# Optimization experiments

Measured on AMD Instinct MI355X. Metric: run time of the kernel, lower is better.

## Reference

```python
import jax, jax.numpy as jnp
import numpy as np

DECAY = 0.99
EPS = 1e-06


def setup_inputs() -> dict:
    key = jax.random.key(0)
    k1, k2, k3 = jax.random.split(key, 3)
    B, S, D, K = 8, 8192, 256, 2048
    x = jax.random.normal(k1, (B, S, D), dtype=jnp.float32)
    embed = jax.random.normal(k2, (K, D), dtype=jnp.float32)
    cluster_size = jnp.ones((K,), dtype=jnp.float32)
    embed_avg = jax.random.normal(k3, (K, D), dtype=jnp.float32)
    return {"x": x, "embed": embed, "cluster_size": cluster_size, "embed_avg": embed_avg}


def reference(x, embed, cluster_size, embed_avg):
    # x: [B, S, D]; embed/embed_avg: [K, D]; cluster_size: [K]
    B, S, D = x.shape
    K = embed.shape[0]
    xf = x.reshape(-1, D)  # [N, D]
    dist = (
        jnp.sum(xf * xf, axis=1, keepdims=True)
        - 2.0 * (xf @ embed.T)
        + jnp.sum(embed * embed, axis=1)
    )
    embed_ind_flat = jnp.argmin(dist, axis=-1)  # [N]
    quantize = embed[embed_ind_flat].reshape(B, S, D)
    embed_ind = embed_ind_flat.reshape(B, S)

    # EMA updates (training branch). one_hot.sum(0) == per-code counts,
    # one_hot.T @ x == per-code feature sums; use segment_sum (no NxK one-hot).
    counts = jax.ops.segment_sum(
        jnp.ones((B * S,), dtype=jnp.float32), embed_ind_flat, num_segments=K
    )
    embed_sum = jax.ops.segment_sum(xf, embed_ind_flat, num_segments=K)  # [K, D]
    new_cluster_size = cluster_size * DECAY + (1.0 - DECAY) * counts
    new_embed_avg = embed_avg * DECAY + (1.0 - DECAY) * embed_sum
    total = new_cluster_size.sum()
    smoothed = (new_cluster_size + EPS) / (total + EPS * K) * total  # laplace smoothing
    new_embed = new_embed_avg / smoothed[:, None]
    return quantize, embed_ind, new_cluster_size, new_embed_avg, new_embed
```

## Files before the change

kernel.cpp:

```cpp
#include <hip/hip_runtime.h>
#include <hip/hip_fp16.h>
#include <float.h>

#define DECAY 0.99f
#define OMD   0.01f
#define EPSF  1e-6f

constexpr int Bb = 8, Ss = 8192, Dd = 256, Kk = 2048;
constexpr int Nn = Bb * Ss;

constexpr long OUT_QUANT = 0;
constexpr long OUT_IND   = (long)Nn * Dd;
constexpr long OUT_NCS   = OUT_IND + Nn;
constexpr long OUT_NEA   = OUT_NCS + Kk;
constexpr long OUT_NE    = OUT_NEA + (long)Kk * Dd;

constexpr long WS_COUNTS = 0;
constexpr long WS_TOTAL  = 2048;
constexpr long WS_EE     = 2112;
constexpr long WS_BIG    = 4160;
constexpr int  PARTS     = 8;
constexpr int  CODES     = 8;

typedef __attribute__((ext_vector_type(8))) short short8;
typedef __attribute__((ext_vector_type(8))) _Float16 half8;
typedef __attribute__((ext_vector_type(4))) float floatx4;

#define WINDOW 0.5f

__device__ __forceinline__ void gl_lds(const ushort* g, ushort* l)
{
    __builtin_amdgcn_global_load_lds(
        (const __attribute__((address_space(1))) void*)g,
        (__attribute__((address_space(3))) void*)l,
        16, 0, 0);
}

__device__ __forceinline__ ushort f2h(float v)
{
    __half h = __float2half(v);
    return *(ushort*)&h;
}

__global__ __launch_bounds__(256) void convert_x_kernel(
    const float* __restrict__ x, ushort* __restrict__ x_h)
{
    long base = ((long)blockIdx.x * 256 + threadIdx.x) * 8;
    float4 a = *(const float4*)&x[base];
    float4 b = *(const float4*)&x[base + 4];
    short8 h;
    h[0] = (short)f2h(a.x); h[1] = (short)f2h(a.y);
    h[2] = (short)f2h(a.z); h[3] = (short)f2h(a.w);
    h[4] = (short)f2h(b.x); h[5] = (short)f2h(b.y);
    h[6] = (short)f2h(b.z); h[7] = (short)f2h(b.w);
    *(short8*)&x_h[base] = h;
}

__global__ __launch_bounds__(256) void convert_e_kernel(
    const float* __restrict__ embed, ushort* __restrict__ e_h,
    float* __restrict__ ee)
{
    int row  = blockIdx.x * 4 + (threadIdx.x >> 6);
    int lane = threadIdx.x & 63;
    long base = (long)row * Dd + lane * 4;
    float4 v = *(const float4*)&embed[base];
    float s = v.x * v.x + v.y * v.y + v.z * v.z + v.w * v.w;
    ushort4 h;
    h.x = f2h(v.x); h.y = f2h(v.y); h.z = f2h(v.z); h.w = f2h(v.w);
    *(ushort4*)&e_h[base] = h;
    #pragma unroll
    for (int off = 32; off >= 1; off >>= 1)
        s += __shfl_xor(s, off, 64);
    if (lane == 0) ee[row] = s;
}

__global__ __attribute__((amdgpu_waves_per_eu(2, 2))) __launch_bounds__(256)
void pass1_kernel(
    const ushort* __restrict__ x_h, const ushort* __restrict__ e_h,
    const float* __restrict__ ee, float* __restrict__ ind_out,
    int* __restrict__ qbase)
{
    __shared__ __attribute__((aligned(16))) ushort ah[128 * 64];
    __shared__ __attribute__((aligned(16))) ushort bh[256 * 64];
    __shared__ float  redv[2][128];
    __shared__ float  red2[2][128];
    __shared__ int    redi[2][128];

    const int tid  = threadIdx.x;
    const int lane = tid & 63;
    const int quad = lane >> 4;
    const int l15  = lane & 15;
    const int w    = tid >> 6;
    const int wy   = w >> 1;
    const int wx   = w & 1;
    const long row0 = (long)blockIdx.x * 128;

    const int rloc   = lane >> 3;
    const int cchunk = (lane & 7) ^ rloc;
    const int gcoff  = rloc * 256 + cchunk * 8;

    const int s7 = l15 & 7;

    float bestv[16], best2v[16];
    int   besti[16];
    #pragma unroll
    for (int i = 0; i < 16; ++i) { bestv[i] = FLT_MAX; best2v[i] = FLT_MAX; besti[i] = 0; }

    for (int ct = 0; ct < Kk / 256; ++ct) {
        floatx4 acc[4][8];
        #pragma unroll
        for (int rt = 0; rt < 4; ++rt)
            #pragma unroll
            for (int jt = 0; jt < 8; ++jt)
                acc[rt][jt] = (floatx4){0.f, 0.f, 0.f, 0.f};

        const long brow = (long)ct * 256;

        for (int kc = 0; kc < 4; ++kc) {
            const int kcol = kc * 64;

            __syncthreads();
            #pragma unroll
            for (int i = 0; i < 4; ++i) {
                const int u = w + 4 * i;
                gl_lds(&x_h[((row0 + u * 8) << 8) + kcol + gcoff], &ah[u * 512]);
            }
            #pragma unroll
            for (int i = 0; i < 8; ++i) {
                const int u = w + 4 * i;
                gl_lds(&e_h[((brow + u * 8) << 8) + kcol + gcoff], &bh[u * 512]);
            }
            __syncthreads();

            #pragma unroll
            for (int ks = 0; ks < 2; ++ks) {
                const int cterm = (((ks * 4 + quad) ^ s7) * 8);
                half8 af[4];
                #pragma unroll
                for (int rt = 0; rt < 4; ++rt)
                    af[rt] = *(const half8*)&ah[((wy * 64 + rt * 16 + l15) << 6) + cterm];
                #pragma unroll
                for (int jt = 0; jt < 8; ++jt) {
                    half8 bf = *(const half8*)&bh[((wx * 128 + jt * 16 + l15) << 6) + cterm];
                    #pragma unroll
                    for (int rt = 0; rt < 4; ++rt)
                        acc[rt][jt] = __builtin_amdgcn_mfma_f32_16x16x32_f16(
                            af[rt], bf, acc[rt][jt], 0, 0, 0);
                }
            }
        }

        #pragma unroll
        for (int jt = 0; jt < 8; ++jt) {
            int c = ct * 256 + wx * 128 + jt * 16 + l15;
            float eec = ee[c];
            #pragma unroll
            for (int rt = 0; rt < 4; ++rt) {
                #pragma unroll
                for (int reg = 0; reg < 4; ++reg) {
                    float s = eec - 2.0f * acc[rt][jt][reg];
                    int slot = rt * 4 + reg;
                    if (s < bestv[slot]) {
                        best2v[slot] = bestv[slot];
                        bestv[slot] = s; besti[slot] = c;
                    } else {
                        best2v[slot] = fminf(best2v[slot], s);
                    }
                }
            }
        }
    }

    #pragma unroll
    for (int slot = 0; slot < 16; ++slot) {
        float bv = bestv[slot]; int bi = besti[slot]; float b2 = best2v[slot];
        #pragma unroll
        for (int off = 8; off >= 1; off >>= 1) {
            float ov  = __shfl_xor(bv, off, 16);
            int   oi  = __shfl_xor(bi, off, 16);
            float ov2 = __shfl_xor(b2, off, 16);
            float nm2 = fminf(fminf(b2, ov2), fmaxf(bv, ov));
            if (ov < bv) { bv = ov; bi = oi; }
            b2 = nm2;
        }
        bestv[slot] = bv; besti[slot] = bi; best2v[slot] = b2;
    }

    if (l15 == 0) {
        #pragma unroll
        for (int rt = 0; rt < 4; ++rt)
            #pragma unroll
            for (int reg = 0; reg < 4; ++reg) {
                int rloc2 = wy * 64 + rt * 16 + quad * 4 + reg;
                int slot = rt * 4 + reg;
                redv[wx][rloc2] = bestv[slot];
                red2[wx][rloc2] = best2v[slot];
                redi[wx][rloc2] = besti[slot];
            }
    }
    __syncthreads();
    if (tid < 128) {
        float v0 = redv[0][tid], v1 = redv[1][tid];
        float s0 = red2[0][tid], s1 = red2[1][tid];
        float m1, m2; int mi;
        if (v0 <= v1) { m1 = v0; mi = redi[0][tid]; m2 = fminf(fminf(s0, s1), v1); }
        else          { m1 = v1; mi = redi[1][tid]; m2 = fminf(fminf(s0, s1), v0); }
        long rowAbs = row0 + tid;
        ind_out[rowAbs] = (float)mi;
        if (m2 - m1 <= WINDOW) {
            int q = atomicAdd(qbase, 1);
            qbase[1 + q] = (int)rowAbs;
        }
    }
}

constexpr int RB = 8;
__global__ __launch_bounds__(256) void pass2_kernel(
    const float* __restrict__ x, const float* __restrict__ embed,
    const float* __restrict__ ee, const int* __restrict__ qbase,
    float* __restrict__ ind_out)
{
    __shared__ float xs[RB][256];
    __shared__ float sv[RB][256];
    __shared__ int   si[RB][256];
    const int tid = threadIdx.x;
    const int count = qbase[0];

    for (int q0 = blockIdx.x * RB; q0 < count; q0 += gridDim.x * RB) {
        const int nr = (count - q0 < RB) ? (count - q0) : RB;
        __syncthreads();
        for (int r = 0; r < nr; ++r)
            xs[r][tid] = x[(long)qbase[1 + q0 + r] * Dd + tid];
        __syncthreads();

        float bv[RB]; int bi[RB];
        #pragma unroll
        for (int r = 0; r < RB; ++r) { bv[r] = FLT_MAX; bi[r] = 0; }

        for (int i = 0; i < Kk / 256; ++i) {
            const int c = i * 256 + tid;
            const float4* er = (const float4*)&embed[(long)c * Dd];
            float dot[RB];
            #pragma unroll
            for (int r = 0; r < RB; ++r) dot[r] = 0.0f;
            for (int d = 0; d < Dd / 4; ++d) {
                float4 e4 = er[d];
                #pragma unroll
                for (int r = 0; r < RB; ++r) {
                    float4 x4 = *(const float4*)&xs[r][d * 4];
                    dot[r] += e4.x * x4.x + e4.y * x4.y + e4.z * x4.z + e4.w * x4.w;
                }
            }
            float eec = ee[c];
            #pragma unroll
            for (int r = 0; r < RB; ++r) {
                float s = eec - 2.0f * dot[r];
                if (s < bv[r]) { bv[r] = s; bi[r] = c; }
            }
        }

        #pragma unroll
        for (int r = 0; r < RB; ++r) { sv[r][tid] = bv[r]; si[r][tid] = bi[r]; }
        __syncthreads();
        for (int off = 128; off >= 1; off >>= 1) {
            if (tid < off) {
                #pragma unroll
                for (int r = 0; r < RB; ++r) {
                    float v2 = sv[r][tid + off]; int i2 = si[r][tid + off];
                    if (v2 < sv[r][tid] || (v2 == sv[r][tid] && i2 < si[r][tid])) {
                        sv[r][tid] = v2; si[r][tid] = i2;
                    }
                }
            }
            __syncthreads();
        }
        if (tid < nr)
            ind_out[qbase[1 + q0 + tid]] = (float)si[tid][0];
        __syncthreads();
    }
}

__global__ __launch_bounds__(256) void quant_gather_kernel(
    const float* __restrict__ embed, const float* __restrict__ ind_f,
    float* __restrict__ quant)
{
    long row  = (long)blockIdx.x * 4 + (threadIdx.x >> 6);
    int  lane = threadIdx.x & 63;
    int  idx  = (int)ind_f[row];
    float4 ev = *(const float4*)&embed[(long)idx * Dd + lane * 4];
    *(float4*)&quant[row * Dd + lane * 4] = ev;
}

template <int USE_ATOMIC>
__global__ __launch_bounds__(256) void segsum_kernel(
    const float* __restrict__ x, const float* __restrict__ ind_f,
    float* __restrict__ dst, float* __restrict__ counts)
{
    __shared__ float part[CODES][4][256];
    __shared__ float cnt_l[CODES][4];
    const int tid  = threadIdx.x;
    const int w    = tid >> 6;
    const int lane = tid & 63;
    const int k0   = (blockIdx.x >> 3) * CODES;
    const int s    = blockIdx.x & 7;

    constexpr int STRIP = Nn / PARTS;
    constexpr int WAVE_ROWS = STRIP / 4;
    const int base0 = s * STRIP + w * WAVE_ROWS;

    float4 acc[CODES];
    int    cnt[CODES];
    #pragma unroll
    for (int c = 0; c < CODES; ++c) { acc[c] = (float4){0.f,0.f,0.f,0.f}; cnt[c] = 0; }

    for (int win = 0; win < WAVE_ROWS; win += 64) {
        int idx = (int)ind_f[base0 + win + lane];
        unsigned rel = (unsigned)(idx - k0);
        unsigned long long m = __ballot(rel < (unsigned)CODES);
        while (m) {
            int l = __ffsll((unsigned long long)m) - 1;
            m &= m - 1;
            int code = __shfl((int)rel, l, 64);
            long row = base0 + win + l;
            float4 v = *(const float4*)&x[row * Dd + lane * 4];
            switch (code) {
                case 0: acc[0].x+=v.x; acc[0].y+=v.y; acc[0].z+=v.z; acc[0].w+=v.w; cnt[0]++; break;
                case 1: acc[1].x+=v.x; acc[1].y+=v.y; acc[1].z+=v.z; acc[1].w+=v.w; cnt[1]++; break;
                case 2: acc[2].x+=v.x; acc[2].y+=v.y; acc[2].z+=v.z; acc[2].w+=v.w; cnt[2]++; break;
                case 3: acc[3].x+=v.x; acc[3].y+=v.y; acc[3].z+=v.z; acc[3].w+=v.w; cnt[3]++; break;
                case 4: acc[4].x+=v.x; acc[4].y+=v.y; acc[4].z+=v.z; acc[4].w+=v.w; cnt[4]++; break;
                case 5: acc[5].x+=v.x; acc[5].y+=v.y; acc[5].z+=v.z; acc[5].w+=v.w; cnt[5]++; break;
                case 6: acc[6].x+=v.x; acc[6].y+=v.y; acc[6].z+=v.z; acc[6].w+=v.w; cnt[6]++; break;
                case 7: acc[7].x+=v.x; acc[7].y+=v.y; acc[7].z+=v.z; acc[7].w+=v.w; cnt[7]++; break;
            }
        }
    }

    #pragma unroll
    for (int c = 0; c < CODES; ++c) {
        *(float4*)&part[c][w][lane * 4] = acc[c];
        if (lane == 0) cnt_l[c][w] = (float)cnt[c];
    }
    __syncthreads();

    #pragma unroll
    for (int c = 0; c < CODES; ++c) {
        float sum = part[c][0][tid] + part[c][1][tid] + part[c][2][tid] + part[c][3][tid];
        if (USE_ATOMIC) {
            if (sum != 0.0f) atomicAdd(&dst[(long)(k0 + c) * Dd + tid], sum);
        } else {
            dst[((long)s * Kk + (k0 + c)) * Dd + tid] = sum;
        }
    }
    if (tid < CODES)
        atomicAdd(&counts[k0 + tid],
                  cnt_l[tid][0] + cnt_l[tid][1] + cnt_l[tid][2] + cnt_l[tid][3]);
}

__global__ __launch_bounds__(256) void ema_cs_kernel(
    const float* __restrict__ cs, const float* __restrict__ counts,
    float* __restrict__ ncs, float* __restrict__ total_ws)
{
    __shared__ float red[256];
    int tid = threadIdx.x;
    float s = 0.0f;
    #pragma unroll
    for (int i = 0; i < 8; ++i) {
        int k = tid + i * 256;
        float v = cs[k] * DECAY + OMD * counts[k];
        ncs[k] = v;
        s += v;
    }
    red[tid] = s;
    __syncthreads();
    #pragma unroll
    for (int off = 128; off >= 1; off >>= 1) {
        if (tid < off) red[tid] += red[tid + off];
        __syncthreads();
    }
    if (tid == 0) total_ws[0] = red[0];
}

__global__ __launch_bounds__(256) void nea_ne_kernel(
    const float* __restrict__ ea, const float* __restrict__ partials,
    int nparts, const float* __restrict__ ncs, const float* __restrict__ total_ws,
    float* __restrict__ nea, float* __restrict__ ne)
{
    long g = ((long)blockIdx.x * 256 + threadIdx.x) * 4;
    int  k = (int)(g >> 8);
    int  d = (int)(g & 255);

    float4 sv = {0.f, 0.f, 0.f, 0.f};
    for (int p = 0; p < nparts; ++p) {
        float4 pv = *(const float4*)&partials[((long)p * Kk + k) * Dd + d];
        sv.x += pv.x; sv.y += pv.y; sv.z += pv.z; sv.w += pv.w;
    }

    float4 av = *(const float4*)&ea[g];
    float4 out_nea;
    out_nea.x = av.x * DECAY + OMD * sv.x;
    out_nea.y = av.y * DECAY + OMD * sv.y;
    out_nea.z = av.z * DECAY + OMD * sv.z;
    out_nea.w = av.w * DECAY + OMD * sv.w;
    *(float4*)&nea[g] = out_nea;

    float total = total_ws[0];
    float sm = (ncs[k] + EPSF) / (total + EPSF * (float)Kk) * total;
    float inv = 1.0f / sm;
    float4 out_ne;
    out_ne.x = out_nea.x * inv;
    out_ne.y = out_nea.y * inv;
    out_ne.z = out_nea.z * inv;
    out_ne.w = out_nea.w * inv;
    *(float4*)&ne[g] = out_ne;
}

extern "C" void kernel_launch(void* const* d_in, const int* in_sizes, int n_in,
                              void* d_out, int out_size, void* d_ws, size_t ws_size,
                              hipStream_t stream)
{
    const float* x     = (const float*)d_in[0];
    const float* embed = (const float*)d_in[1];
    const float* cs    = (const float*)d_in[2];
    const float* ea    = (const float*)d_in[3];

    float* out   = (float*)d_out;
    float* quant = out + OUT_QUANT;
    float* ind_f = out + OUT_IND;
    float* ncs   = out + OUT_NCS;
    float* nea   = out + OUT_NEA;
    float* ne    = out + OUT_NE;

    float* ws     = (float*)d_ws;
    float* counts = ws + WS_COUNTS;
    float* total  = ws + WS_TOTAL;
    float* ee     = ws + WS_EE;
    float* big    = ws + WS_BIG;

    ushort* x_h = (ushort*)(out + OUT_QUANT);
    ushort* e_h = (ushort*)(out + OUT_NEA);
    int*    qb  = (int*)(out + OUT_NE);

    const size_t need_partials =
        (size_t)(WS_BIG + (long)PARTS * Kk * Dd) * sizeof(float) + 1024;
    const bool use_ws_partials = ws_size >= need_partials;

    hipMemsetAsync(counts, 0, Kk * sizeof(float), stream);
    hipMemsetAsync(qb, 0, sizeof(int), stream);
    if (!use_ws_partials)
        hipMemsetAsync(big, 0, (size_t)Kk * Dd * sizeof(float), stream);

    convert_x_kernel<<<(Nn * Dd / 8) / 256, 256, 0, stream>>>(x, x_h);
    convert_e_kernel<<<Kk / 4, 256, 0, stream>>>(embed, e_h, ee);
    pass1_kernel<<<Nn / 128, 256, 0, stream>>>(x_h, e_h, ee, ind_f, qb);
    pass2_kernel<<<512, 256, 0, stream>>>(x, embed, ee, qb, ind_f);
    quant_gather_kernel<<<Nn / 4, 256, 0, stream>>>(embed, ind_f, quant);
    if (use_ws_partials)
        segsum_kernel<0><<<(Kk / CODES) * PARTS, 256, 0, stream>>>(x, ind_f, big, counts);
    else
        segsum_kernel<1><<<(Kk / CODES) * PARTS, 256, 0, stream>>>(x, ind_f, big, counts);
    ema_cs_kernel<<<1, 256, 0, stream>>>(cs, counts, ncs, total);
    nea_ne_kernel<<<(Kk * Dd / 4) / 256, 256, 0, stream>>>(
        ea, big, use_ws_partials ? PARTS : 1, ncs, total, nea, ne);
}
```

Measured before the change: 478.9 us.

## Fuse x fp16 conversion into pass1 and stream codebook from global

Removes the separate x-to-fp16 conversion kernel by having pass1 load its 64-row x tile directly as fp32, convert it, and keep the full 256-wide tile resident in swizzled LDS. The codebook operand is no longer staged through LDS; each wave reads its 64 codes' fp16 fragments straight from global memory. Each wave now owns a 64-code slice instead of a 2x2 split, and the final argmin reduction merges four waves. This drops an extra pass over x and the inner-loop barriers, but makes B-operand loads uncached global reads repeated by every block, roughly doubles the block count, and removes the waves-per-eu hint.

Measured after the change: 543.0 us. +13.4%, slower.

```diff
diff --git a/kernel.cpp b/kernel.cpp
--- a/kernel.cpp
+++ b/kernel.cpp
@@ -28,32 +28,10 @@
 
 #define WINDOW 0.5f
 
-__device__ __forceinline__ void gl_lds(const ushort* g, ushort* l)
-{
-    __builtin_amdgcn_global_load_lds(
-        (const __attribute__((address_space(1))) void*)g,
-        (__attribute__((address_space(3))) void*)l,
-        16, 0, 0);
-}
-
 __device__ __forceinline__ ushort f2h(float v)
 {
     __half h = __float2half(v);
     return *(ushort*)&h;
-}
-
-__global__ __launch_bounds__(256) void convert_x_kernel(
-    const float* __restrict__ x, ushort* __restrict__ x_h)
-{
-    long base = ((long)blockIdx.x * 256 + threadIdx.x) * 8;
-    float4 a = *(const float4*)&x[base];
-    float4 b = *(const float4*)&x[base + 4];
-    short8 h;
-    h[0] = (short)f2h(a.x); h[1] = (short)f2h(a.y);
-    h[2] = (short)f2h(a.z); h[3] = (short)f2h(a.w);
-    h[4] = (short)f2h(b.x); h[5] = (short)f2h(b.y);
-    h[6] = (short)f2h(b.z); h[7] = (short)f2h(b.w);
-    *(short8*)&x_h[base] = h;
 }
 
 __global__ __launch_bounds__(256) void convert_e_kernel(
@@ -74,32 +52,35 @@
     if (lane == 0) ee[row] = s;
 }
 
-__global__ __attribute__((amdgpu_waves_per_eu(2, 2))) __launch_bounds__(256)
-void pass1_kernel(
-    const ushort* __restrict__ x_h, const ushort* __restrict__ e_h,
+__global__ __launch_bounds__(256) void pass1_kernel(
+    const float* __restrict__ x, const ushort* __restrict__ e_h,
     const float* __restrict__ ee, float* __restrict__ ind_out,
     int* __restrict__ qbase)
 {
-    __shared__ __attribute__((aligned(16))) ushort ah[128 * 64];
-    __shared__ __attribute__((aligned(16))) ushort bh[256 * 64];
-    __shared__ float  redv[2][128];
-    __shared__ float  red2[2][128];
-    __shared__ int    redi[2][128];
+    __shared__ __attribute__((aligned(16))) ushort as[64 * 256];
+    __shared__ float redv[4][64];
+    __shared__ float red2[4][64];
+    __shared__ int   redi[4][64];
 
     const int tid  = threadIdx.x;
     const int lane = tid & 63;
     const int quad = lane >> 4;
     const int l15  = lane & 15;
     const int w    = tid >> 6;
-    const int wy   = w >> 1;
-    const int wx   = w & 1;
-    const long row0 = (long)blockIdx.x * 128;
-
-    const int rloc   = lane >> 3;
-    const int cchunk = (lane & 7) ^ rloc;
-    const int gcoff  = rloc * 256 + cchunk * 8;
-
-    const int s7 = l15 & 7;
+    const long row0 = (long)blockIdx.x * 64;
+
+    #pragma unroll
+    for (int i = 0; i < 16; ++i) {
+        int li = i * 256 + tid;
+        int r  = li >> 6;
+        int c  = (li & 63) * 4;
+        float4 v = *(const float4*)&x[row0 * Dd + (long)li * 4];
+        ushort4 h;
+        h.x = f2h(v.x); h.y = f2h(v.y); h.z = f2h(v.z); h.w = f2h(v.w);
+        int slot = (c >> 3) ^ (r & 7);
+        *(ushort4*)&as[r * 256 + slot * 8 + (c & 7)] = h;
+    }
+    __syncthreads();
 
     float bestv[16], best2v[16];
     int   besti[16];
@@ -107,52 +88,39 @@
     for (int i = 0; i < 16; ++i) { bestv[i] = FLT_MAX; best2v[i] = FLT_MAX; besti[i] = 0; }
 
     for (int ct = 0; ct < Kk / 256; ++ct) {
-        floatx4 acc[4][8];
+        floatx4 acc[4][4];
         #pragma unroll
         for (int rt = 0; rt < 4; ++rt)
             #pragma unroll
-            for (int jt = 0; jt < 8; ++jt)
+            for (int jt = 0; jt < 4; ++jt)
                 acc[rt][jt] = (floatx4){0.f, 0.f, 0.f, 0.f};
 
-        const long brow = (long)ct * 256;
-
-        for (int kc = 0; kc < 4; ++kc) {
-            const int kcol = kc * 64;
-
-            __syncthreads();
-            #pragma unroll
-            for (int i = 0; i < 4; ++i) {
-                const int u = w + 4 * i;
-                gl_lds(&x_h[((row0 + u * 8) << 8) + kcol + gcoff], &ah[u * 512]);
-            }
-            #pragma unroll
-            for (int i = 0; i < 8; ++i) {
-                const int u = w + 4 * i;
-                gl_lds(&e_h[((brow + u * 8) << 8) + kcol + gcoff], &bh[u * 512]);
-            }
-            __syncthreads();
-
-            #pragma unroll
-            for (int ks = 0; ks < 2; ++ks) {
-                const int cterm = (((ks * 4 + quad) ^ s7) * 8);
-                half8 af[4];
+        const int cbase = ct * 256 + w * 64 + l15;
+
+        #pragma unroll
+        for (int ks = 0; ks < 8; ++ks) {
+            half8 af[4];
+            #pragma unroll
+            for (int rt = 0; rt < 4; ++rt) {
+                int chunk = ks * 4 + quad;
+                af[rt] = *(const half8*)&as[(rt * 16 + l15) * 256 +
+                                            ((chunk ^ (l15 & 7)) << 3)];
+            }
+            #pragma unroll
+            for (int jt = 0; jt < 4; ++jt) {
+                const ushort* bp = &e_h[((long)(cbase + jt * 16) << 8) +
+                                        ks * 32 + quad * 8];
+                half8 bf = *(const half8*)bp;
                 #pragma unroll
                 for (int rt = 0; rt < 4; ++rt)
-                    af[rt] = *(const half8*)&ah[((wy * 64 + rt * 16 + l15) << 6) + cterm];
-                #pragma unroll
-                for (int jt = 0; jt < 8; ++jt) {
-                    half8 bf = *(const half8*)&bh[((wx * 128 + jt * 16 + l15) << 6) + cterm];
-                    #pragma unroll
-                    for (int rt = 0; rt < 4; ++rt)
-                        acc[rt][jt] = __builtin_amdgcn_mfma_f32_16x16x32_f16(
-                            af[rt], bf, acc[rt][jt], 0, 0, 0);
-                }
-            }
-        }
-
-        #pragma unroll
-        for (int jt = 0; jt < 8; ++jt) {
-            int c = ct * 256 + wx * 128 + jt * 16 + l15;
+                    acc[rt][jt] = __builtin_amdgcn_mfma_f32_16x16x32_f16(
+                        af[rt], bf, acc[rt][jt], 0, 0, 0);
+            }
+        }
+
+        #pragma unroll
+        for (int jt = 0; jt < 4; ++jt) {
+            int c = ct * 256 + w * 64 + jt * 16 + l15;
             float eec = ee[c];
             #pragma unroll
             for (int rt = 0; rt < 4; ++rt) {
@@ -191,20 +159,31 @@
         for (int rt = 0; rt < 4; ++rt)
             #pragma unroll
             for (int reg = 0; reg < 4; ++reg) {
-                int rloc2 = wy * 64 + rt * 16 + quad * 4 + reg;
+                int rloc = rt * 16 + quad * 4 + reg;
                 int slot = rt * 4 + reg;
-                redv[wx][rloc2] = bestv[slot];
-                red2[wx][rloc2] = best2v[slot];
-                redi[wx][rloc2] = besti[slot];
+                redv[w][rloc] = bestv[slot];
+                red2[w][rloc] = best2v[slot];
+                redi[w][rloc] = besti[slot];
             }
     }
     __syncthreads();
-    if (tid < 128) {
-        float v0 = redv[0][tid], v1 = redv[1][tid];
-        float s0 = red2[0][tid], s1 = red2[1][tid];
-        float m1, m2; int mi;
-        if (v0 <= v1) { m1 = v0; mi = redi[0][tid]; m2 = fminf(fminf(s0, s1), v1); }
-        else          { m1 = v1; mi = redi[1][tid]; m2 = fminf(fminf(s0, s1), v0); }
+
+    if (tid < 64) {
+        float v[4], s2[4]; int ix[4];
+        #pragma unroll
+        for (int p = 0; p < 4; ++p) {
+            v[p] = redv[p][tid]; s2[p] = red2[p][tid]; ix[p] = redi[p][tid];
+        }
+        float m1 = v[0]; int mi = ix[0]; int arg = 0;
+        #pragma unroll
+        for (int p = 1; p < 4; ++p)
+            if (v[p] < m1) { m1 = v[p]; mi = ix[p]; arg = p; }
+        float m2 = FLT_MAX;
+        #pragma unroll
+        for (int p = 0; p < 4; ++p) {
+            m2 = fminf(m2, s2[p]);
+            if (p != arg) m2 = fminf(m2, v[p]);
+        }
         long rowAbs = row0 + tid;
         ind_out[rowAbs] = (float)mi;
         if (m2 - m1 <= WINDOW) {
@@ -437,7 +416,6 @@
     float* ee     = ws + WS_EE;
     float* big    = ws + WS_BIG;
 
-    ushort* x_h = (ushort*)(out + OUT_QUANT);
     ushort* e_h = (ushort*)(out + OUT_NEA);
     int*    qb  = (int*)(out + OUT_NE);
 
@@ -450,9 +428,8 @@
     if (!use_ws_partials)
         hipMemsetAsync(big, 0, (size_t)Kk * Dd * sizeof(float), stream);
 
-    convert_x_kernel<<<(Nn * Dd / 8) / 256, 256, 0, stream>>>(x, x_h);
     convert_e_kernel<<<Kk / 4, 256, 0, stream>>>(embed, e_h, ee);
-    pass1_kernel<<<Nn / 128, 256, 0, stream>>>(x_h, e_h, ee, ind_f, qb);
+    pass1_kernel<<<Nn / 64, 256, 0, stream>>>(x, e_h, ee, ind_f, qb);
     pass2_kernel<<<512, 256, 0, stream>>>(x, embed, ee, qb, ind_f);
     quant_gather_kernel<<<Nn / 4, 256, 0, stream>>>(embed, ind_f, quant);
     if (use_ws_partials)
```

## Fuse x fp16 conversion and quantize gather into double-buffered pass1

Applied to the files above, without the earlier changes.

Drops the separate x-to-fp16 conversion kernel: pass1 now loads fp32 x directly, converts in registers and writes fp16 tiles to LDS. The K loop is restructured into 32-wide chunks with double-buffered LDS, prefetching the next chunk while the current one runs on the MFMAs, with one barrier per chunk instead of two. The quantize gather moves into the pass1 epilogue, with pass2 rewriting rows it corrects, and the qbase reset folds into convert_e. Together these remove a full fp16 round trip of x through memory and two kernel launches, at the cost of more conversion work and register pressure inside the GEMM loop.

After: 491.0 us. +2.5%, slower.

```diff
diff --git a/kernel.cpp b/kernel.cpp
--- a/kernel.cpp
+++ b/kernel.cpp
@@ -42,24 +42,11 @@
     return *(ushort*)&h;
 }
 
-__global__ __launch_bounds__(256) void convert_x_kernel(
-    const float* __restrict__ x, ushort* __restrict__ x_h)
-{
-    long base = ((long)blockIdx.x * 256 + threadIdx.x) * 8;
-    float4 a = *(const float4*)&x[base];
-    float4 b = *(const float4*)&x[base + 4];
-    short8 h;
-    h[0] = (short)f2h(a.x); h[1] = (short)f2h(a.y);
-    h[2] = (short)f2h(a.z); h[3] = (short)f2h(a.w);
-    h[4] = (short)f2h(b.x); h[5] = (short)f2h(b.y);
-    h[6] = (short)f2h(b.z); h[7] = (short)f2h(b.w);
-    *(short8*)&x_h[base] = h;
-}
-
 __global__ __launch_bounds__(256) void convert_e_kernel(
     const float* __restrict__ embed, ushort* __restrict__ e_h,
-    float* __restrict__ ee)
-{
+    float* __restrict__ ee, int* __restrict__ qbase)
+{
+    if (blockIdx.x == 0 && threadIdx.x == 0) qbase[0] = 0;
     int row  = blockIdx.x * 4 + (threadIdx.x >> 6);
     int lane = threadIdx.x & 63;
     long base = (long)row * Dd + lane * 4;
@@ -76,15 +63,17 @@
 
 __global__ __attribute__((amdgpu_waves_per_eu(2, 2))) __launch_bounds__(256)
 void pass1_kernel(
-    const ushort* __restrict__ x_h, const ushort* __restrict__ e_h,
-    const float* __restrict__ ee, float* __restrict__ ind_out,
+    const float* __restrict__ x, const ushort* __restrict__ e_h,
+    const float* __restrict__ embed, const float* __restrict__ ee,
+    float* __restrict__ ind_out, float* __restrict__ quant,
     int* __restrict__ qbase)
 {
-    __shared__ __attribute__((aligned(16))) ushort ah[128 * 64];
-    __shared__ __attribute__((aligned(16))) ushort bh[256 * 64];
-    __shared__ float  redv[2][128];
-    __shared__ float  red2[2][128];
-    __shared__ int    redi[2][128];
+    __shared__ __attribute__((aligned(16))) ushort ah[2][128 * 32];
+    __shared__ __attribute__((aligned(16))) ushort bh[2][256 * 32];
+    __shared__ float redv[2][128];
+    __shared__ float red2[2][128];
+    __shared__ int   redi[2][128];
+    __shared__ int   idxs[128];
 
     const int tid  = threadIdx.x;
     const int lane = tid & 63;
@@ -95,18 +84,61 @@
     const int wx   = w & 1;
     const long row0 = (long)blockIdx.x * 128;
 
-    const int rloc   = lane >> 3;
-    const int cchunk = (lane & 7) ^ rloc;
+    const int rloc   = lane >> 2;
+    const int cchunk = (lane & 3) ^ ((rloc >> 1) & 3);
     const int gcoff  = rloc * 256 + cchunk * 8;
 
-    const int s7 = l15 & 7;
+    const int a_r    = lane >> 2;
+    const int a_c    = lane & 3;
+    const int a_slot = a_c ^ ((lane >> 3) & 3);
+
+    const int sread = (l15 >> 1) & 3;
+    const int aoff0 = ((wy * 64 + l15) << 5) + ((quad ^ sread) << 3);
+    const int boff0 = ((wx * 128 + l15) << 5) + ((quad ^ sread) << 3);
+
+#define STAGE_B(b, ctn, kcn) do {                                          \
+    const long bb = (((long)(ctn) * 256) << 8) + (kcn) * 32 + gcoff;       \
+    gl_lds(&e_h[bb + ((long)w << 12)],        &bh[b][w * 512]);            \
+    gl_lds(&e_h[bb + ((long)(w + 4) << 12)],  &bh[b][(w + 4) * 512]);      \
+    gl_lds(&e_h[bb + ((long)(w + 8) << 12)],  &bh[b][(w + 8) * 512]);      \
+    gl_lds(&e_h[bb + ((long)(w + 12) << 12)], &bh[b][(w + 12) * 512]);     \
+} while (0)
+
+#define STAGE_A_LOAD(kcn) do {                                             \
+    const long ar = ((row0 + w * 16 + a_r) << 8) + (kcn) * 32 + a_c * 8;   \
+    const long br = ((row0 + (w + 4) * 16 + a_r) << 8) + (kcn) * 32 + a_c * 8; \
+    pa0 = *(const float4*)&x[ar]; pa1 = *(const float4*)&x[ar + 4];        \
+    pb0 = *(const float4*)&x[br]; pb1 = *(const float4*)&x[br + 4];        \
+} while (0)
+
+#define STAGE_A_WRITE(b) do {                                              \
+    half8 h0, h1;                                                          \
+    h0[0]=(_Float16)pa0.x; h0[1]=(_Float16)pa0.y;                          \
+    h0[2]=(_Float16)pa0.z; h0[3]=(_Float16)pa0.w;                          \
+    h0[4]=(_Float16)pa1.x; h0[5]=(_Float16)pa1.y;                          \
+    h0[6]=(_Float16)pa1.z; h0[7]=(_Float16)pa1.w;                          \
+    h1[0]=(_Float16)pb0.x; h1[1]=(_Float16)pb0.y;                          \
+    h1[2]=(_Float16)pb0.z; h1[3]=(_Float16)pb0.w;                          \
+    h1[4]=(_Float16)pb1.x; h1[5]=(_Float16)pb1.y;                          \
+    h1[6]=(_Float16)pb1.z; h1[7]=(_Float16)pb1.w;                          \
+    *(half8*)&ah[b][(w * 16 + a_r) * 32 + a_slot * 8] = h0;                \
+    *(half8*)&ah[b][((w + 4) * 16 + a_r) * 32 + a_slot * 8] = h1;          \
+} while (0)
+
+    float4 pa0, pa1, pb0, pb1;
 
     float bestv[16], best2v[16];
     int   besti[16];
     #pragma unroll
     for (int i = 0; i < 16; ++i) { bestv[i] = FLT_MAX; best2v[i] = FLT_MAX; besti[i] = 0; }
 
-    for (int ct = 0; ct < Kk / 256; ++ct) {
+    STAGE_A_LOAD(0);
+    STAGE_B(0, 0, 0);
+    STAGE_A_WRITE(0);
+    __syncthreads();
+
+    int buf = 0;
+    for (int ct = 0; ct < 8; ++ct) {
         floatx4 acc[4][8];
         #pragma unroll
         for (int rt = 0; rt < 4; ++rt)
@@ -114,40 +146,31 @@
             for (int jt = 0; jt < 8; ++jt)
                 acc[rt][jt] = (floatx4){0.f, 0.f, 0.f, 0.f};
 
-        const long brow = (long)ct * 256;
-
-        for (int kc = 0; kc < 4; ++kc) {
-            const int kcol = kc * 64;
-
-            __syncthreads();
-            #pragma unroll
-            for (int i = 0; i < 4; ++i) {
-                const int u = w + 4 * i;
-                gl_lds(&x_h[((row0 + u * 8) << 8) + kcol + gcoff], &ah[u * 512]);
-            }
-            #pragma unroll
-            for (int i = 0; i < 8; ++i) {
-                const int u = w + 4 * i;
-                gl_lds(&e_h[((brow + u * 8) << 8) + kcol + gcoff], &bh[u * 512]);
-            }
-            __syncthreads();
-
-            #pragma unroll
-            for (int ks = 0; ks < 2; ++ks) {
-                const int cterm = (((ks * 4 + quad) ^ s7) * 8);
-                half8 af[4];
+        for (int kc = 0; kc < 8; ++kc) {
+            const int p  = ct * 8 + kc;
+            const int pn = p + 1;
+            const bool more = (pn < 64);
+            if (more) {
+                STAGE_A_LOAD(pn & 7);
+                STAGE_B(buf ^ 1, pn >> 3, pn & 7);
+            }
+
+            half8 af[4];
+            #pragma unroll
+            for (int rt = 0; rt < 4; ++rt)
+                af[rt] = *(const half8*)&ah[buf][aoff0 + (rt << 9)];
+            #pragma unroll
+            for (int jt = 0; jt < 8; ++jt) {
+                half8 bf = *(const half8*)&bh[buf][boff0 + (jt << 9)];
                 #pragma unroll
                 for (int rt = 0; rt < 4; ++rt)
-                    af[rt] = *(const half8*)&ah[((wy * 64 + rt * 16 + l15) << 6) + cterm];
-                #pragma unroll
-                for (int jt = 0; jt < 8; ++jt) {
-                    half8 bf = *(const half8*)&bh[((wx * 128 + jt * 16 + l15) << 6) + cterm];
-                    #pragma unroll
-                    for (int rt = 0; rt < 4; ++rt)
-                        acc[rt][jt] = __builtin_amdgcn_mfma_f32_16x16x32_f16(
-                            af[rt], bf, acc[rt][jt], 0, 0, 0);
-                }
-            }
+                    acc[rt][jt] = __builtin_amdgcn_mfma_f32_16x16x32_f16(
+                        af[rt], bf, acc[rt][jt], 0, 0, 0);
+            }
+
+            if (more) STAGE_A_WRITE(buf ^ 1);
+            __syncthreads();
+            buf ^= 1;
         }
 
         #pragma unroll
@@ -170,6 +193,9 @@
             }
         }
     }
+#undef STAGE_B
+#undef STAGE_A_LOAD
+#undef STAGE_A_WRITE
 
     #pragma unroll
     for (int slot = 0; slot < 16; ++slot) {
@@ -191,11 +217,11 @@
         for (int rt = 0; rt < 4; ++rt)
             #pragma unroll
             for (int reg = 0; reg < 4; ++reg) {
-                int rloc2 = wy * 64 + rt * 16 + quad * 4 + reg;
+                int rl = wy * 64 + rt * 16 + quad * 4 + reg;
                 int slot = rt * 4 + reg;
-                redv[wx][rloc2] = bestv[slot];
-                red2[wx][rloc2] = best2v[slot];
-                redi[wx][rloc2] = besti[slot];
+                redv[wx][rl] = bestv[slot];
+                red2[wx][rl] = best2v[slot];
+                redi[wx][rl] = besti[slot];
             }
     }
     __syncthreads();
@@ -207,10 +233,20 @@
         else          { m1 = v1; mi = redi[1][tid]; m2 = fminf(fminf(s0, s1), v0); }
         long rowAbs = row0 + tid;
         ind_out[rowAbs] = (float)mi;
+        idxs[tid] = mi;
         if (m2 - m1 <= WINDOW) {
             int q = atomicAdd(qbase, 1);
             qbase[1 + q] = (int)rowAbs;
         }
+    }
+    __syncthreads();
+
+    #pragma unroll
+    for (int rr = 0; rr < 32; ++rr) {
+        int r = w * 32 + rr;
+        int idx = idxs[r];
+        float4 ev = *(const float4*)&embed[(long)idx * Dd + lane * 4];
+        *(float4*)&quant[(row0 + r) * Dd + lane * 4] = ev;
     }
 }
 
@@ -218,7 +254,7 @@
 __global__ __launch_bounds__(256) void pass2_kernel(
     const float* __restrict__ x, const float* __restrict__ embed,
     const float* __restrict__ ee, const int* __restrict__ qbase,
-    float* __restrict__ ind_out)
+    float* __restrict__ ind_out, float* __restrict__ quant)
 {
     __shared__ float xs[RB][256];
     __shared__ float sv[RB][256];
@@ -276,19 +312,13 @@
         }
         if (tid < nr)
             ind_out[qbase[1 + q0 + tid]] = (float)si[tid][0];
+        for (int r = 0; r < nr; ++r) {
+            int code = si[r][0];
+            long row = qbase[1 + q0 + r];
+            quant[row * Dd + tid] = embed[(long)code * Dd + tid];
+        }
         __syncthreads();
     }
-}
-
-__global__ __launch_bounds__(256) void quant_gather_kernel(
-    const float* __restrict__ embed, const float* __restrict__ ind_f,
-    float* __restrict__ quant)
-{
-    long row  = (long)blockIdx.x * 4 + (threadIdx.x >> 6);
-    int  lane = threadIdx.x & 63;
-    int  idx  = (int)ind_f[row];
-    float4 ev = *(const float4*)&embed[(long)idx * Dd + lane * 4];
-    *(float4*)&quant[row * Dd + lane * 4] = ev;
 }
 
 template <int USE_ATOMIC>
@@ -437,7 +467,6 @@
     float* ee     = ws + WS_EE;
     float* big    = ws + WS_BIG;
 
-    ushort* x_h = (ushort*)(out + OUT_QUANT);
     ushort* e_h = (ushort*)(out + OUT_NEA);
     int*    qb  = (int*)(out + OUT_NE);
 
@@ -446,15 +475,12 @@
     const bool use_ws_partials = ws_size >= need_partials;
 
     hipMemsetAsync(counts, 0, Kk * sizeof(float), stream);
-    hipMemsetAsync(qb, 0, sizeof(int), stream);
     if (!use_ws_partials)
         hipMemsetAsync(big, 0, (size_t)Kk * Dd * sizeof(float), stream);
 
-    convert_x_kernel<<<(Nn * Dd / 8) / 256, 256, 0, stream>>>(x, x_h);
-    convert_e_kernel<<<Kk / 4, 256, 0, stream>>>(embed, e_h, ee);
-    pass1_kernel<<<Nn / 128, 256, 0, stream>>>(x_h, e_h, ee, ind_f, qb);
-    pass2_kernel<<<512, 256, 0, stream>>>(x, embed, ee, qb, ind_f);
-    quant_gather_kernel<<<Nn / 4, 256, 0, stream>>>(embed, ind_f, quant);
+    convert_e_kernel<<<Kk / 4, 256, 0, stream>>>(embed, e_h, ee, qb);
+    pass1_kernel<<<Nn / 128, 256, 0, stream>>>(x, e_h, embed, ee, ind_f, quant, qb);
+    pass2_kernel<<<512, 256, 0, stream>>>(x, embed, ee, qb, ind_f, quant);
     if (use_ws_partials)
         segsum_kernel<0><<<(Kk / CODES) * PARTS, 256, 0, stream>>>(x, ind_f, big, counts);
     else
```
